# Optimization experiments

Measured on AMD Instinct MI355X. Metric: run time of the kernel, lower is better.

## Reference

```python
import jax, jax.numpy as jnp
import numpy as np

N, E, C_IN, C_OUT, K, D_D = 50000, 800000, 16, 64, 3, 7


def setup_inputs() -> dict:
    key = jax.random.key(0)
    ks = jax.random.split(key, 10)
    s = 0.05
    x = jax.random.normal(ks[0], (N, C_IN), jnp.float32)
    edge_index = jax.random.randint(ks[1], (2, E), 0, N, dtype=jnp.int64)
    edge_weight = jax.random.uniform(ks[2], (E,), jnp.float32)
    h0 = jax.random.normal(ks[3], (N, C_OUT), jnp.float32)
    # stacked ChebConv params: gate order [z, r, h]
    Wx = jax.random.normal(ks[4], (3, K, C_IN, C_OUT), jnp.float32) * s
    Wh = jax.random.normal(ks[5], (3, K, C_OUT, C_OUT), jnp.float32) * s
    bx = jax.random.normal(ks[6], (3, C_OUT), jnp.float32) * s
    bh = jax.random.normal(ks[7], (3, C_OUT), jnp.float32) * s
    Wlin = jax.random.normal(ks[8], (C_OUT, D_D), jnp.float32) * s
    blin = jax.random.normal(ks[9], (D_D,), jnp.float32) * s
    return dict(x=x, edge_index=edge_index, edge_weight=edge_weight, h0=h0,
                Wx=Wx, Wh=Wh, bx=bx, bh=bh, Wlin=Wlin, blin=blin)


def _norm(src, dst, edge_weight, n):
    # ChebConv sym normalization with lambda_max=2:
    # L_sym = I - D^-1/2 A D^-1/2;  L_tilde = 2L/lambda_max - I = -D^-1/2 A D^-1/2
    w = jnp.where(src == dst, 0.0, edge_weight)  # remove self loops
    deg = jax.ops.segment_sum(w, src, num_segments=n)
    dinv = jnp.where(deg > 0, 1.0 / jnp.sqrt(deg), 0.0)
    return -dinv[src] * w * dinv[dst]


def _cheb(t, W, b, src, dst, nw, n):
    # K-hop Chebyshev recursion: Tx_{k+1} = 2*L~*Tx_k - Tx_{k-1}
    prop = lambda v: jax.ops.segment_sum(nw[:, None] * v[src], dst, num_segments=n)
    Tx0 = t
    out = Tx0 @ W[0]
    Tx1 = prop(Tx0)
    out = out + Tx1 @ W[1]
    for k in range(2, W.shape[0]):
        Tx2 = 2.0 * prop(Tx1) - Tx0
        out = out + Tx2 @ W[k]
        Tx0, Tx1 = Tx1, Tx2
    return out + b


def reference(x, edge_index, edge_weight, h0, Wx, Wh, bx, bh, Wlin, blin):
    n = x.shape[0]
    src, dst = edge_index[0], edge_index[1]
    nw = _norm(src, dst, edge_weight, n)
    z = jax.nn.sigmoid(_cheb(x, Wx[0], bx[0], src, dst, nw, n)
                       + _cheb(h0, Wh[0], bh[0], src, dst, nw, n))
    r = jax.nn.sigmoid(_cheb(x, Wx[1], bx[1], src, dst, nw, n)
                       + _cheb(h0, Wh[1], bh[1], src, dst, nw, n))
    htil = jnp.tanh(_cheb(x, Wx[2], bx[2], src, dst, nw, n)
                    + _cheb(h0 * r, Wh[2], bh[2], src, dst, nw, n))
    h = z * h0 + (1.0 - z) * htil
    y = jax.nn.relu(h) @ Wlin + blin
    return (jax.lax.stop_gradient(h), y)
```

## Files before the change

kernel.cpp:

```cpp
#include <hip/hip_runtime.h>

constexpr int NN = 50000;
constexpr int NE = 800000;
constexpr int CI = 16;
constexpr int CO = 64;
constexpr int DD = 7;
constexpr int NXCD = 8;

typedef __bf16 bf16x8 __attribute__((ext_vector_type(8)));
typedef float  f32x4  __attribute__((ext_vector_type(4)));
typedef float  f32x2  __attribute__((ext_vector_type(2)));

__device__ inline float blo(unsigned u) { return __uint_as_float(u << 16); }
__device__ inline float bhi(unsigned u) { return __uint_as_float(u & 0xffff0000u); }

__device__ inline unsigned xcc_id() {
    unsigned v;
    asm volatile("s_getreg_b32 %0, hwreg(HW_REG_XCC_ID)" : "=s"(v));
    return v & 7;
}
__device__ inline int l2_add_ret(int* p, int v) {
    return __hip_atomic_fetch_add(p, v, __ATOMIC_RELAXED, __HIP_MEMORY_SCOPE_WORKGROUP);
}
__device__ inline void l2_add_f(float* p, float v) {
    __hip_atomic_fetch_add(p, v, __ATOMIC_RELAXED, __HIP_MEMORY_SCOPE_WORKGROUP);
}

__device__ inline void acc8_fp8(float acc[8], float w, uint2 u) {
    f32x2 c;
    c = __builtin_amdgcn_cvt_pk_f32_fp8(u.x, false); acc[0] += w * c[0]; acc[1] += w * c[1];
    c = __builtin_amdgcn_cvt_pk_f32_fp8(u.x, true);  acc[2] += w * c[0]; acc[3] += w * c[1];
    c = __builtin_amdgcn_cvt_pk_f32_fp8(u.y, false); acc[4] += w * c[0]; acc[5] += w * c[1];
    c = __builtin_amdgcn_cvt_pk_f32_fp8(u.y, true);  acc[6] += w * c[0]; acc[7] += w * c[1];
}
__device__ inline uint2 pack_fp8x8(const float o[8]) {
    int t0 = __builtin_amdgcn_cvt_pk_fp8_f32(o[0], o[1], 0, false);
    t0 = __builtin_amdgcn_cvt_pk_fp8_f32(o[2], o[3], t0, true);
    int t1 = __builtin_amdgcn_cvt_pk_fp8_f32(o[4], o[5], 0, false);
    t1 = __builtin_amdgcn_cvt_pk_fp8_f32(o[6], o[7], t1, true);
    uint2 r; r.x = (unsigned)t0; r.y = (unsigned)t1; return r;
}
__device__ inline unsigned char fp8_of(float v) {
    return (unsigned char)(__builtin_amdgcn_cvt_pk_fp8_f32(v, v, 0, false) & 0xff);
}


constexpr int EB = (NE + 255) / 256;
constexpr int XOCT = NN * CI / 8;
constexpr int HOCT = NN * CO / 8;
constexpr int CB = (XOCT + HOCT + 255) / 256;

__global__ void __launch_bounds__(256) k_deg_cast_prep(
    const int* __restrict__ src, const int* __restrict__ dst, const float* __restrict__ ew,
    float* __restrict__ deg8, int* __restrict__ count8, uint2* __restrict__ erec,
    const float* __restrict__ x, const float* __restrict__ h0,
    __bf16* __restrict__ x_bf, __bf16* __restrict__ h0_bf, unsigned char* __restrict__ h0_f8,
    const float* __restrict__ Wx, const float* __restrict__ Wh,
    const float* __restrict__ bx, const float* __restrict__ bh,
    bf16x8* __restrict__ BfragZR, bf16x8* __restrict__ BfragHT, float* __restrict__ biasC) {
    int b = blockIdx.x;
    if (b < EB) {
        int e = b * 256 + threadIdx.x;
        if (e >= NE) return;
        int s = src[e], d = dst[e];
        float w = (s == d) ? 0.f : ew[e];
        unsigned xc = xcc_id();
        l2_add_f(&deg8[xc * NN + s], w);
        int rk = l2_add_ret(&count8[xc * NN + d], 1);
        __bf16 wb = (__bf16)w;
        unsigned wu = (unsigned)__builtin_bit_cast(unsigned short, wb);
        erec[e] = make_uint2((unsigned)s | ((unsigned)d << 16),
                             ((unsigned)rk & 0xff) | (xc << 8) | (wu << 16));
    } else if (b < EB + CB) {
        int t = (b - EB) * 256 + threadIdx.x;
        if (t < XOCT) {
            const float* sp = x + (size_t)t * 8;
            float4 a = *(const float4*)sp;
            float4 c = *(const float4*)(sp + 4);
            bf16x8 o;
            o[0] = (__bf16)a.x; o[1] = (__bf16)a.y; o[2] = (__bf16)a.z; o[3] = (__bf16)a.w;
            o[4] = (__bf16)c.x; o[5] = (__bf16)c.y; o[6] = (__bf16)c.z; o[7] = (__bf16)c.w;
            *(bf16x8*)(x_bf + (size_t)t * 8) = o;
        } else if (t < XOCT + HOCT) {
            int u = t - XOCT;
            const float* sp = h0 + (size_t)u * 8;
            float4 a = *(const float4*)sp;
            float4 c = *(const float4*)(sp + 4);
            bf16x8 o;
            o[0] = (__bf16)a.x; o[1] = (__bf16)a.y; o[2] = (__bf16)a.z; o[3] = (__bf16)a.w;
            o[4] = (__bf16)c.x; o[5] = (__bf16)c.y; o[6] = (__bf16)c.z; o[7] = (__bf16)c.w;
            *(bf16x8*)(h0_bf + (size_t)u * 8) = o;
            float f[8] = {a.x, a.y, a.z, a.w, c.x, c.y, c.z, c.w};
            *(uint2*)(h0_f8 + (size_t)u * 8) = pack_fp8x8(f);
        }
    } else {
        int tid = (b - EB - CB) * 256 + threadIdx.x;
        if (tid < 6144) {
            int e = tid, gate, n, kk, l;
            if (e < 4096) {
                int t = e >> 9, rem = e & 511;
                kk = rem >> 6; l = rem & 63;
                n = t * 16 + (l & 15);
                gate = n >> 6;
            } else {
                int e2 = e - 4096;
                int t = e2 >> 9, rem = e2 & 511;
                kk = rem >> 6; l = rem & 63;
                n = t * 16 + (l & 15);
                gate = 2;
            }
            int co = n & 63;
            int k0 = kk * 32 + (l >> 4) * 8;
            bf16x8 f;
#pragma unroll
            for (int j = 0; j < 8; j++) {
                int k = k0 + j;
                float w = 0.f;
                if (k < 48) {
                    int kb = k >> 4, ci = k & 15;
                    const float* Wg = Wx + gate * 3 * 16 * 64;
                    float w0 = Wg[(kb * 16 + ci) * 64 + co];
                    if (kb == 0)      w = w0 - Wg[(2 * 16 + ci) * 64 + co];
                    else if (kb == 1) w = w0;
                    else              w = 2.f * w0;
                } else if (k < 240) {
                    int kh = k - 48, kb = kh >> 6, ci = kh & 63;
                    const float* Wg = Wh + gate * 3 * 64 * 64;
                    float w0 = Wg[(kb * 64 + ci) * 64 + co];
                    if (kb == 0)      w = w0 - Wg[(2 * 64 + ci) * 64 + co];
                    else if (kb == 1) w = w0;
                    else              w = 2.f * w0;
                }
                f[j] = (__bf16)w;
            }
            if (e < 4096) BfragZR[e] = f; else BfragHT[e - 4096] = f;
        } else if (tid < 6144 + 192) {
            int i = tid - 6144;
            biasC[i] = bx[i] + bh[i];
        }
    }
}


__global__ void k_scan1(const int* __restrict__ count8, int* __restrict__ S, int* __restrict__ bsums) {
    __shared__ int ts[256];
    int tid = threadIdx.x;
    int base = blockIdx.x * 1024;
    int vals[4]; int s = 0;
#pragma unroll
    for (int j = 0; j < 4; j++) {
        int idx = base + tid * 4 + j;
        int v = 0;
        if (idx < NN) {
#pragma unroll
            for (int xc = 0; xc < NXCD; xc++) v += count8[xc * NN + idx];
        }
        s += v; vals[j] = s;
    }
    ts[tid] = s;
    __syncthreads();
    for (int off = 1; off < 256; off <<= 1) {
        int v = (tid >= off) ? ts[tid - off] : 0;
        __syncthreads();
        ts[tid] += v;
        __syncthreads();
    }
    int prev = (tid > 0) ? ts[tid - 1] : 0;
#pragma unroll
    for (int j = 0; j < 4; j++) {
        int idx = base + tid * 4 + j;
        if (idx < NN) S[idx] = vals[j] + prev;
    }
    if (tid == 255) bsums[blockIdx.x] = ts[255];
}

__global__ void k_scan23(const int* __restrict__ S, const int* __restrict__ bsums,
                         const int* __restrict__ count8, const float* __restrict__ deg8,
                         int* __restrict__ rowptr, int* __restrict__ off8,
                         float* __restrict__ dinv) {
    int i = blockIdx.x * 256 + threadIdx.x;
    if (i >= NN) return;
    int chunk = blockIdx.x >> 2;
    int pre = 0;
    for (int j = 0; j < chunk; j++) pre += bsums[j];
    int tot = S[i] + pre;
    rowptr[i + 1] = tot;
    if (i == 0) rowptr[0] = 0;
    int c[NXCD]; int ctot = 0;
#pragma unroll
    for (int xc = 0; xc < NXCD; xc++) { c[xc] = count8[xc * NN + i]; ctot += c[xc]; }
    int run = tot - ctot;
#pragma unroll
    for (int xc = 0; xc < NXCD; xc++) { off8[xc * NN + i] = run; run += c[xc]; }
    float dsum = 0.f;
#pragma unroll
    for (int xc = 0; xc < NXCD; xc++) dsum += deg8[xc * NN + i];
    dinv[i] = (dsum > 0.f) ? (1.f / sqrtf(dsum)) : 0.f;
}

__global__ void k_place(const uint2* __restrict__ erec, const float* __restrict__ dinv,
                        const int* __restrict__ off8, unsigned* __restrict__ csr_ew) {
    int e = blockIdx.x * 256 + threadIdx.x;
    if (e >= NE) return;
    uint2 r = erec[e];
    int s = r.x & 0xffff, d = r.x >> 16;
    unsigned rk = r.y & 0xff, xc = (r.y >> 8) & 7;
    float w = bhi(r.y);
    float wp = dinv[s] * w;
    __bf16 wb = (__bf16)wp;
    unsigned short ub = __builtin_bit_cast(unsigned short, wb);
    csr_ew[off8[xc * NN + d] + rk] = (unsigned)s | ((unsigned)ub << 16);
}


__device__ inline void prop64_body(int n, int lane,
                                   const unsigned char* __restrict__ v8,
                                   const float* __restrict__ dinv,
                                   const int* __restrict__ rowptr,
                                   const unsigned* __restrict__ ew,
                                   __bf16* __restrict__ out_bf,
                                   unsigned char* __restrict__ out_f8) {
    int j = lane >> 3, cg = lane & 7;
    int beg = rowptr[n], end = rowptr[n + 1];
    float acc[8] = {0.f, 0.f, 0.f, 0.f, 0.f, 0.f, 0.f, 0.f};
    for (int e = beg + j; e < end; e += 8) {
        unsigned p = ew[e];
        float w = bhi(p);
        int s = p & 0xffff;
        uint2 u = *(const uint2*)(v8 + (size_t)s * 64 + cg * 8);
        acc8_fp8(acc, w, u);
    }
#pragma unroll
    for (int m = 8; m <= 32; m <<= 1) {
#pragma unroll
        for (int i = 0; i < 8; i++) acc[i] += __shfl_xor(acc[i], m, 64);
    }
    if (lane < 8) {
        float f = -dinv[n];
        float o[8];
#pragma unroll
        for (int i = 0; i < 8; i++) o[i] = f * acc[i];
        bf16x8 st;
#pragma unroll
        for (int i = 0; i < 8; i++) st[i] = (__bf16)o[i];
        *(bf16x8*)(out_bf + (size_t)n * 64 + lane * 8) = st;
        if (out_f8) *(uint2*)(out_f8 + (size_t)n * 64 + lane * 8) = pack_fp8x8(o);
    }
}

__device__ inline void prop16_body(int n, int lane,
                                   const __bf16* __restrict__ v,
                                   const float* __restrict__ dinv,
                                   const int* __restrict__ rowptr,
                                   const unsigned* __restrict__ ew, __bf16* __restrict__ out) {
    int j = lane >> 1, cg = lane & 1;
    int beg = rowptr[n], end = rowptr[n + 1];
    float acc[8] = {0.f, 0.f, 0.f, 0.f, 0.f, 0.f, 0.f, 0.f};
    for (int e = beg + j; e < end; e += 32) {
        unsigned p = ew[e];
        float w = bhi(p);
        int s = p & 0xffff;
        uint4 u = *(const uint4*)((const char*)v + ((size_t)s * 32 + cg * 16));
        acc[0] += w * blo(u.x); acc[1] += w * bhi(u.x);
        acc[2] += w * blo(u.y); acc[3] += w * bhi(u.y);
        acc[4] += w * blo(u.z); acc[5] += w * bhi(u.z);
        acc[6] += w * blo(u.w); acc[7] += w * bhi(u.w);
    }
#pragma unroll
    for (int m = 2; m <= 32; m <<= 1) {
#pragma unroll
        for (int i = 0; i < 8; i++) acc[i] += __shfl_xor(acc[i], m, 64);
    }
    if (lane < 2) {
        float f = -dinv[n];
        bf16x8 st;
#pragma unroll
        for (int i = 0; i < 8; i++) st[i] = (__bf16)(f * acc[i]);
        *(bf16x8*)(out + (size_t)n * 16 + lane * 8) = st;
    }
}

__global__ void __launch_bounds__(256) k_stage(
    const unsigned char* __restrict__ vh8, const __bf16* __restrict__ vx,
    const float* __restrict__ dinv,
    const int* __restrict__ rowptr, const unsigned* __restrict__ ew,
    __bf16* __restrict__ outh_bf, unsigned char* __restrict__ outh_f8,
    __bf16* __restrict__ outx) {
    int gw = blockIdx.x * 4 + (threadIdx.x >> 6);
    int lane = threadIdx.x & 63;
    if (gw < NN) prop64_body(gw, lane, vh8, dinv, rowptr, ew, outh_bf, outh_f8);
    else if (gw < 2 * NN) prop16_body(gw - NN, lane, vx, dinv, rowptr, ew, outx);
}

__global__ void __launch_bounds__(256) k_prop64(
    const unsigned char* __restrict__ v8, const float* __restrict__ dinv,
    const int* __restrict__ rowptr, const unsigned* __restrict__ ew,
    __bf16* __restrict__ out_bf, unsigned char* __restrict__ out_f8) {
    int n = blockIdx.x * 4 + (threadIdx.x >> 6);
    if (n >= NN) return;
    prop64_body(n, threadIdx.x & 63, v8, dinv, rowptr, ew, out_bf, out_f8);
}


__device__ inline bf16x8 load_a_bf(int c, int m,
                                   const __bf16* __restrict__ xb, const __bf16* __restrict__ t1,
                                   const __bf16* __restrict__ t2, const __bf16* __restrict__ hb,
                                   const __bf16* __restrict__ h1, const __bf16* __restrict__ h2) {
    if (c >= 30) {
        bf16x8 a;
#pragma unroll
        for (int j = 0; j < 8; j++) a[j] = (__bf16)0.f;
        return a;
    }
    if (c < 6) {
        const __bf16* base = (c < 2) ? xb : ((c < 4) ? t1 : t2);
        return *(const bf16x8*)(base + (size_t)m * 16 + (c & 1) * 8);
    }
    int d = c - 6;
    const __bf16* base = (d < 8) ? hb : ((d < 16) ? h1 : h2);
    return *(const bf16x8*)(base + (size_t)m * 64 + (d & 7) * 8);
}

__global__ void __launch_bounds__(256) k_mfma_zr(
    const __bf16* __restrict__ xb, const __bf16* __restrict__ t1, const __bf16* __restrict__ t2,
    const __bf16* __restrict__ hb, const __bf16* __restrict__ h1, const __bf16* __restrict__ h2,
    const bf16x8* __restrict__ Bfrag, const float* __restrict__ biasC,
    __bf16* __restrict__ z_bf, __bf16* __restrict__ hr_bf, unsigned char* __restrict__ hr_f8) {
    int wv = (blockIdx.x * 256 + threadIdx.x) >> 6;
    if (wv >= NN / 16) return;
    int lane = threadIdx.x & 63;
    int q = lane >> 4, r16 = lane & 15;
    int ma = wv * 16 + r16;
    f32x4 acc[8];
#pragma unroll
    for (int t = 0; t < 8; t++) acc[t] = (f32x4){0.f, 0.f, 0.f, 0.f};
#pragma unroll
    for (int kk = 0; kk < 8; kk++) {
        bf16x8 a = load_a_bf(kk * 4 + q, ma, xb, t1, t2, hb, h1, h2);
#pragma unroll
        for (int t = 0; t < 8; t++)
            acc[t] = __builtin_amdgcn_mfma_f32_16x16x32_bf16(a, Bfrag[(t * 8 + kk) * 64 + lane], acc[t], 0, 0, 0);
    }
    int mbase = wv * 16 + q * 4;
#pragma unroll
    for (int t = 0; t < 8; t++) {
        int co = t * 16 + r16;
        float bias = biasC[co];
        int col = co & 63;
#pragma unroll
        for (int reg = 0; reg < 4; reg++) {
            int mm = mbase + reg;
            float p = acc[t][reg] + bias;
            float s = 1.f / (1.f + __expf(-p));
            if (t < 4) z_bf[(size_t)mm * 64 + col] = (__bf16)s;
            else {
                float hrv = s * (float)hb[(size_t)mm * 64 + col];
                hr_bf[(size_t)mm * 64 + col] = (__bf16)hrv;
                hr_f8[(size_t)mm * 64 + col] = fp8_of(hrv);
            }
        }
    }
}

__global__ void __launch_bounds__(256) k_mfma_ht(
    const __bf16* __restrict__ xb, const __bf16* __restrict__ t1, const __bf16* __restrict__ t2,
    const __bf16* __restrict__ hrb, const __bf16* __restrict__ r1, const __bf16* __restrict__ r2,
    const bf16x8* __restrict__ Bfrag, const float* __restrict__ biasC,
    const __bf16* __restrict__ z_bf, const float* __restrict__ h0,
    const float* __restrict__ Wlin, const float* __restrict__ blin,
    float* __restrict__ hout, float* __restrict__ yout) {
    int wv = (blockIdx.x * 256 + threadIdx.x) >> 6;
    if (wv >= NN / 16) return;
    int lane = threadIdx.x & 63;
    int q = lane >> 4, r16 = lane & 15;
    int ma = wv * 16 + r16;
    f32x4 acc[4];
#pragma unroll
    for (int t = 0; t < 4; t++) acc[t] = (f32x4){0.f, 0.f, 0.f, 0.f};
#pragma unroll
    for (int kk = 0; kk < 8; kk++) {
        bf16x8 a = load_a_bf(kk * 4 + q, ma, xb, t1, t2, hrb, r1, r2);
#pragma unroll
        for (int t = 0; t < 4; t++)
            acc[t] = __builtin_amdgcn_mfma_f32_16x16x32_bf16(a, Bfrag[(t * 8 + kk) * 64 + lane], acc[t], 0, 0, 0);
    }
    int mbase = wv * 16 + q * 4;
    float hbuf[4][4];
#pragma unroll
    for (int t = 0; t < 4; t++) {
        int co = t * 16 + r16;
        float bias = biasC[128 + co];
#pragma unroll
        for (int reg = 0; reg < 4; reg++) {
            int mm = mbase + reg;
            float p = acc[t][reg] + bias;
            float htl = tanhf(p);
            float zv = (float)z_bf[(size_t)mm * 64 + co];
            float h0v = h0[(size_t)mm * 64 + co];
            float hn = zv * h0v + (1.f - zv) * htl;
            hout[(size_t)mm * 64 + co] = hn;
            hbuf[t][reg] = hn;
        }
    }
    float ya[4][DD];
#pragma unroll
    for (int reg = 0; reg < 4; reg++)
#pragma unroll
        for (int d = 0; d < DD; d++) ya[reg][d] = 0.f;
#pragma unroll
    for (int t = 0; t < 4; t++) {
        int cb = (t * 16 + r16) * DD;
        float wl[DD];
#pragma unroll
        for (int d = 0; d < DD; d++) wl[d] = Wlin[cb + d];
#pragma unroll
        for (int reg = 0; reg < 4; reg++) {
            float rh = fmaxf(hbuf[t][reg], 0.f);
#pragma unroll
            for (int d = 0; d < DD; d++) ya[reg][d] += rh * wl[d];
        }
    }
#pragma unroll
    for (int m = 1; m <= 8; m <<= 1) {
#pragma unroll
        for (int reg = 0; reg < 4; reg++)
#pragma unroll
            for (int d = 0; d < DD; d++) ya[reg][d] += __shfl_xor(ya[reg][d], m, 64);
    }
    if (r16 < DD) {
        float b = blin[r16];
#pragma unroll
        for (int reg = 0; reg < 4; reg++) {
            float v = (r16 == 0) ? ya[reg][0] : (r16 == 1) ? ya[reg][1] : (r16 == 2) ? ya[reg][2]
                    : (r16 == 3) ? ya[reg][3] : (r16 == 4) ? ya[reg][4] : (r16 == 5) ? ya[reg][5]
                    : ya[reg][6];
            yout[(size_t)(mbase + reg) * DD + r16] = v + b;
        }
    }
}


extern "C" void kernel_launch(void* const* d_in, const int* in_sizes, int n_in,
                              void* d_out, int out_size, void* d_ws, size_t ws_size,
                              hipStream_t stream) {
    (void)in_sizes; (void)n_in; (void)out_size; (void)ws_size;
    const float* x    = (const float*)d_in[0];
    const int*   eidx = (const int*)d_in[1];
    const float* ew   = (const float*)d_in[2];
    const float* h0   = (const float*)d_in[3];
    const float* Wx   = (const float*)d_in[4];
    const float* Wh   = (const float*)d_in[5];
    const float* bx   = (const float*)d_in[6];
    const float* bh   = (const float*)d_in[7];
    const float* Wlin = (const float*)d_in[8];
    const float* blin = (const float*)d_in[9];
    const int* src = eidx;
    const int* dst = eidx + NE;

    char* ws = (char*)d_ws;
    size_t off = 0;
    auto alloc = [&](size_t nbytes) -> void* {
        void* p = ws + off;
        off += (nbytes + 255) & ~(size_t)255;
        return p;
    };
    float*  deg8    = (float*)alloc((size_t)NXCD * NN * 4);
    int*    count8  = (int*)alloc((size_t)NXCD * NN * 4);
    int*    off8    = (int*)alloc((size_t)NXCD * NN * 4);
    float*  dinv    = (float*)alloc(NN * 4);
    int*    S       = (int*)alloc(NN * 4);
    int*    rowptr  = (int*)alloc((NN + 1) * 4);
    int*    bsums   = (int*)alloc(64 * 4);
    uint2*  erec    = (uint2*)alloc((size_t)NE * 8);
    unsigned* csr_ew = (unsigned*)alloc((size_t)NE * 4);
    __bf16* x_bf    = (__bf16*)alloc((size_t)NN * CI * 2);
    __bf16* h0_bf   = (__bf16*)alloc((size_t)NN * CO * 2);
    unsigned char* h0_f8 = (unsigned char*)alloc((size_t)NN * CO);
    unsigned char* T1_f8 = (unsigned char*)alloc((size_t)NN * CO);
    unsigned char* hr_f8 = (unsigned char*)alloc((size_t)NN * CO);
    __bf16* Tx1     = (__bf16*)alloc((size_t)NN * CI * 2);
    __bf16* Tx2     = (__bf16*)alloc((size_t)NN * CI * 2);
    __bf16* Th1     = (__bf16*)alloc((size_t)NN * CO * 2);
    __bf16* Th2     = (__bf16*)alloc((size_t)NN * CO * 2);
    __bf16* hr_bf   = (__bf16*)alloc((size_t)NN * CO * 2);
    __bf16* z_bf    = (__bf16*)alloc((size_t)NN * CO * 2);
    bf16x8* BfragZR = (bf16x8*)alloc(4096 * 16);
    bf16x8* BfragHT = (bf16x8*)alloc(2048 * 16);
    float*  biasC   = (float*)alloc(192 * 4);

    float* hout = (float*)d_out;
    float* yout = hout + (size_t)NN * CO;

    constexpr int NB = (NN + 1023) / 1024;
    const int NBLK = (NN + 255) / 256;
    const int PROPB = (NN + 3) / 4;
    const int STAGEB = (2 * NN + 3) / 4;
    const int GEMMB = (NN / 16 * 64 + 255) / 256;

    hipMemsetAsync(deg8, 0, (size_t)NXCD * NN * 4, stream);
    hipMemsetAsync(count8, 0, (size_t)NXCD * NN * 4, stream);

    k_deg_cast_prep<<<EB + CB + 25, 256, 0, stream>>>(
        src, dst, ew, deg8, count8, erec, x, h0, x_bf, h0_bf, h0_f8,
        Wx, Wh, bx, bh, BfragZR, BfragHT, biasC);
    k_scan1<<<NB, 256, 0, stream>>>(count8, S, bsums);
    k_scan23<<<NBLK, 256, 0, stream>>>(S, bsums, count8, deg8, rowptr, off8, dinv);
    k_place<<<EB, 256, 0, stream>>>(erec, dinv, off8, csr_ew);

    k_stage<<<STAGEB, 256, 0, stream>>>(h0_f8, x_bf, dinv, rowptr, csr_ew, Th1, T1_f8, Tx1);
    k_stage<<<STAGEB, 256, 0, stream>>>(T1_f8, Tx1, dinv, rowptr, csr_ew, Th2, nullptr, Tx2);

    k_mfma_zr<<<GEMMB, 256, 0, stream>>>(x_bf, Tx1, Tx2, h0_bf, Th1, Th2,
                                         BfragZR, biasC, z_bf, hr_bf, hr_f8);
    k_prop64<<<PROPB, 256, 0, stream>>>(hr_f8, dinv, rowptr, csr_ew, Th1, T1_f8);
    k_prop64<<<PROPB, 256, 0, stream>>>(T1_f8, dinv, rowptr, csr_ew, Th2, nullptr);
    k_mfma_ht<<<GEMMB, 256, 0, stream>>>(x_bf, Tx1, Tx2, hr_bf, Th1, Th2,
                                         BfragHT, biasC, z_bf, h0, Wlin, blin, hout, yout);
}
```

Measured before the change: 363.4 us.

## Build CSR via two-level bucket sort with LDS histograms instead of global atomics

Replaces the per-XCD global-atomic degree/count pass, multi-kernel scan and placement with a counting sort. Edges are first bucketed by node>>8 using per-block shared-memory histograms, a single scan over the bucket tables, and a scatter. Per-bucket kernels then compute degrees and build rowptr/csr with shared-memory atomics. This removes global atomic contention and the memsets, at the cost of more kernels, extra record arrays (drec/srec) and a serial 1024-thread table scan.

```diff
diff --git a/kernel.cpp b/kernel.cpp
--- a/kernel.cpp
+++ b/kernel.cpp
@@ -5,7 +5,11 @@
 constexpr int CI = 16;
 constexpr int CO = 64;
 constexpr int DD = 7;
-constexpr int NXCD = 8;
+
+constexpr int NBUCK = 196;
+constexpr int EPB   = 4096;
+constexpr int NBLK3 = (NE + EPB - 1) / EPB;
+constexpr int TBL   = NBUCK * NBLK3;
 
 typedef __bf16 bf16x8 __attribute__((ext_vector_type(8)));
 typedef float  f32x4  __attribute__((ext_vector_type(4)));
@@ -13,18 +17,6 @@
 
 __device__ inline float blo(unsigned u) { return __uint_as_float(u << 16); }
 __device__ inline float bhi(unsigned u) { return __uint_as_float(u & 0xffff0000u); }
-
-__device__ inline unsigned xcc_id() {
-    unsigned v;
-    asm volatile("s_getreg_b32 %0, hwreg(HW_REG_XCC_ID)" : "=s"(v));
-    return v & 7;
-}
-__device__ inline int l2_add_ret(int* p, int v) {
-    return __hip_atomic_fetch_add(p, v, __ATOMIC_RELAXED, __HIP_MEMORY_SCOPE_WORKGROUP);
-}
-__device__ inline void l2_add_f(float* p, float v) {
-    __hip_atomic_fetch_add(p, v, __ATOMIC_RELAXED, __HIP_MEMORY_SCOPE_WORKGROUP);
-}
 
 __device__ inline void acc8_fp8(float acc[8], float w, uint2 u) {
     f32x2 c;
@@ -45,34 +37,40 @@
 }
 
 
-constexpr int EB = (NE + 255) / 256;
 constexpr int XOCT = NN * CI / 8;
 constexpr int HOCT = NN * CO / 8;
 constexpr int CB = (XOCT + HOCT + 255) / 256;
 
-__global__ void __launch_bounds__(256) k_deg_cast_prep(
-    const int* __restrict__ src, const int* __restrict__ dst, const float* __restrict__ ew,
-    float* __restrict__ deg8, int* __restrict__ count8, uint2* __restrict__ erec,
+__global__ void __launch_bounds__(256) k_count(
+    const int* __restrict__ src, const int* __restrict__ dst,
+    int* __restrict__ Cd, int* __restrict__ Cs,
     const float* __restrict__ x, const float* __restrict__ h0,
     __bf16* __restrict__ x_bf, __bf16* __restrict__ h0_bf, unsigned char* __restrict__ h0_f8,
     const float* __restrict__ Wx, const float* __restrict__ Wh,
     const float* __restrict__ bx, const float* __restrict__ bh,
     bf16x8* __restrict__ BfragZR, bf16x8* __restrict__ BfragHT, float* __restrict__ biasC) {
     int b = blockIdx.x;
-    if (b < EB) {
-        int e = b * 256 + threadIdx.x;
-        if (e >= NE) return;
-        int s = src[e], d = dst[e];
-        float w = (s == d) ? 0.f : ew[e];
-        unsigned xc = xcc_id();
-        l2_add_f(&deg8[xc * NN + s], w);
-        int rk = l2_add_ret(&count8[xc * NN + d], 1);
-        __bf16 wb = (__bf16)w;
-        unsigned wu = (unsigned)__builtin_bit_cast(unsigned short, wb);
-        erec[e] = make_uint2((unsigned)s | ((unsigned)d << 16),
-                             ((unsigned)rk & 0xff) | (xc << 8) | (wu << 16));
-    } else if (b < EB + CB) {
-        int t = (b - EB) * 256 + threadIdx.x;
+    if (b < NBLK3) {
+        __shared__ int hd[NBUCK], hs[NBUCK];
+        for (int i = threadIdx.x; i < NBUCK; i += 256) { hd[i] = 0; hs[i] = 0; }
+        __syncthreads();
+        int base = b * EPB;
+#pragma unroll
+        for (int k = 0; k < EPB / 256; k++) {
+            int e = base + k * 256 + threadIdx.x;
+            if (e < NE) {
+                int s = src[e], d = dst[e];
+                atomicAdd(&hd[d >> 8], 1);
+                atomicAdd(&hs[s >> 8], 1);
+            }
+        }
+        __syncthreads();
+        for (int i = threadIdx.x; i < NBUCK; i += 256) {
+            Cd[i * NBLK3 + b] = hd[i];
+            Cs[i * NBLK3 + b] = hs[i];
+        }
+    } else if (b < NBLK3 + CB) {
+        int t = (b - NBLK3) * 256 + threadIdx.x;
         if (t < XOCT) {
             const float* sp = x + (size_t)t * 8;
             float4 a = *(const float4*)sp;
@@ -94,7 +92,7 @@
             *(uint2*)(h0_f8 + (size_t)u * 8) = pack_fp8x8(f);
         }
     } else {
-        int tid = (b - EB - CB) * 256 + threadIdx.x;
+        int tid = (b - NBLK3 - CB) * 256 + threadIdx.x;
         if (tid < 6144) {
             int e = tid, gate, n, kk, l;
             if (e < 4096) {
@@ -142,74 +140,124 @@
 }
 
 
-__global__ void k_scan1(const int* __restrict__ count8, int* __restrict__ S, int* __restrict__ bsums) {
-    __shared__ int ts[256];
-    int tid = threadIdx.x;
-    int base = blockIdx.x * 1024;
-    int vals[4]; int s = 0;
-#pragma unroll
-    for (int j = 0; j < 4; j++) {
-        int idx = base + tid * 4 + j;
-        int v = 0;
-        if (idx < NN) {
-#pragma unroll
-            for (int xc = 0; xc < NXCD; xc++) v += count8[xc * NN + idx];
-        }
-        s += v; vals[j] = s;
-    }
-    ts[tid] = s;
+__global__ void __launch_bounds__(1024) k_scan_tables(int* __restrict__ Cd, int* __restrict__ Cs) {
+    int* C = (blockIdx.x == 0) ? Cd : Cs;
+    constexpr int CHUNK = (TBL + 1023) / 1024;
+    __shared__ int part[1024];
+    int t = threadIdx.x;
+    int base = t * CHUNK;
+    int v[CHUNK];
+    int s = 0;
+#pragma unroll
+    for (int j = 0; j < CHUNK; j++) {
+        int idx = base + j;
+        int xv = (idx < TBL) ? C[idx] : 0;
+        v[j] = s;
+        s += xv;
+    }
+    part[t] = s;
+    __syncthreads();
+    for (int off = 1; off < 1024; off <<= 1) {
+        int p = (t >= off) ? part[t - off] : 0;
+        __syncthreads();
+        part[t] += p;
+        __syncthreads();
+    }
+    int tb = (t > 0) ? part[t - 1] : 0;
+#pragma unroll
+    for (int j = 0; j < CHUNK; j++) {
+        int idx = base + j;
+        if (idx < TBL) C[idx] = tb + v[j];
+    }
+}
+
+
+__global__ void __launch_bounds__(256) k_scatter(
+    const int* __restrict__ src, const int* __restrict__ dst, const float* __restrict__ ew,
+    const int* __restrict__ Cd, const int* __restrict__ Cs,
+    uint2* __restrict__ drec, uint2* __restrict__ srec) {
+    __shared__ int cd[NBUCK], cs[NBUCK];
+    int b = blockIdx.x;
+    for (int i = threadIdx.x; i < NBUCK; i += 256) {
+        cd[i] = Cd[i * NBLK3 + b];
+        cs[i] = Cs[i * NBLK3 + b];
+    }
+    __syncthreads();
+    int base = b * EPB;
+#pragma unroll
+    for (int k = 0; k < EPB / 256; k++) {
+        int e = base + k * 256 + threadIdx.x;
+        if (e < NE) {
+            int s = src[e], d = dst[e];
+            float w = (s == d) ? 0.f : ew[e];
+            __bf16 wb = (__bf16)w;
+            unsigned wu = (unsigned)__builtin_bit_cast(unsigned short, wb);
+            int pd = atomicAdd(&cd[d >> 8], 1);
+            drec[pd] = make_uint2((unsigned)s | (wu << 16), (unsigned)(d & 255));
+            int ps = atomicAdd(&cs[s >> 8], 1);
+            srec[ps] = make_uint2((unsigned)(s & 255), __builtin_bit_cast(unsigned, w));
+        }
+    }
+}
+
+
+__global__ void __launch_bounds__(256) k_dinv(
+    const int* __restrict__ Cs, const uint2* __restrict__ srec, float* __restrict__ dinv) {
+    int bkt = blockIdx.x;
+    __shared__ float acc[256];
+    acc[threadIdx.x] = 0.f;
+    __syncthreads();
+    int beg = Cs[bkt * NBLK3];
+    int end = (bkt == NBUCK - 1) ? NE : Cs[(bkt + 1) * NBLK3];
+    for (int i = beg + threadIdx.x; i < end; i += 256) {
+        uint2 r = srec[i];
+        atomicAdd(&acc[r.x], __builtin_bit_cast(float, r.y));
+    }
+    __syncthreads();
+    int node = bkt * 256 + threadIdx.x;
+    if (node < NN) {
+        float dsum = acc[threadIdx.x];
+        dinv[node] = (dsum > 0.f) ? (1.f / sqrtf(dsum)) : 0.f;
+    }
+}
+
+
+__global__ void __launch_bounds__(256) k_build(
+    const int* __restrict__ Cd, const uint2* __restrict__ drec, const float* __restrict__ dinv,
+    int* __restrict__ rowptr, unsigned* __restrict__ csr_ew) {
+    int bkt = blockIdx.x;
+    __shared__ int cnt[256], sc[256], cur[256];
+    int t = threadIdx.x;
+    cnt[t] = 0;
+    __syncthreads();
+    int beg = Cd[bkt * NBLK3];
+    int end = (bkt == NBUCK - 1) ? NE : Cd[(bkt + 1) * NBLK3];
+    for (int i = beg + t; i < end; i += 256) atomicAdd(&cnt[drec[i].y], 1);
+    __syncthreads();
+    int val = cnt[t];
+    sc[t] = val;
     __syncthreads();
     for (int off = 1; off < 256; off <<= 1) {
-        int v = (tid >= off) ? ts[tid - off] : 0;
+        int p = (t >= off) ? sc[t - off] : 0;
         __syncthreads();
-        ts[tid] += v;
+        sc[t] += p;
         __syncthreads();
     }
-    int prev = (tid > 0) ? ts[tid - 1] : 0;
-#pragma unroll
-    for (int j = 0; j < 4; j++) {
-        int idx = base + tid * 4 + j;
-        if (idx < NN) S[idx] = vals[j] + prev;
-    }
-    if (tid == 255) bsums[blockIdx.x] = ts[255];
-}
-
-__global__ void k_scan23(const int* __restrict__ S, const int* __restrict__ bsums,
-                         const int* __restrict__ count8, const float* __restrict__ deg8,
-                         int* __restrict__ rowptr, int* __restrict__ off8,
-                         float* __restrict__ dinv) {
-    int i = blockIdx.x * 256 + threadIdx.x;
-    if (i >= NN) return;
-    int chunk = blockIdx.x >> 2;
-    int pre = 0;
-    for (int j = 0; j < chunk; j++) pre += bsums[j];
-    int tot = S[i] + pre;
-    rowptr[i + 1] = tot;
-    if (i == 0) rowptr[0] = 0;
-    int c[NXCD]; int ctot = 0;
-#pragma unroll
-    for (int xc = 0; xc < NXCD; xc++) { c[xc] = count8[xc * NN + i]; ctot += c[xc]; }
-    int run = tot - ctot;
-#pragma unroll
-    for (int xc = 0; xc < NXCD; xc++) { off8[xc * NN + i] = run; run += c[xc]; }
-    float dsum = 0.f;
-#pragma unroll
-    for (int xc = 0; xc < NXCD; xc++) dsum += deg8[xc * NN + i];
-    dinv[i] = (dsum > 0.f) ? (1.f / sqrtf(dsum)) : 0.f;
-}
-
-__global__ void k_place(const uint2* __restrict__ erec, const float* __restrict__ dinv,
-                        const int* __restrict__ off8, unsigned* __restrict__ csr_ew) {
-    int e = blockIdx.x * 256 + threadIdx.x;
-    if (e >= NE) return;
-    uint2 r = erec[e];
-    int s = r.x & 0xffff, d = r.x >> 16;
-    unsigned rk = r.y & 0xff, xc = (r.y >> 8) & 7;
-    float w = bhi(r.y);
-    float wp = dinv[s] * w;
-    __bf16 wb = (__bf16)wp;
-    unsigned short ub = __builtin_bit_cast(unsigned short, wb);
-    csr_ew[off8[xc * NN + d] + rk] = (unsigned)s | ((unsigned)ub << 16);
+    int ex = sc[t] - val;
+    int node = bkt * 256 + t;
+    if (node <= NN) rowptr[node] = beg + ex;
+    cur[t] = ex;
+    __syncthreads();
+    for (int i = beg + t; i < end; i += 256) {
+        uint2 r = drec[i];
+        int slot = beg + atomicAdd(&cur[r.y], 1);
+        unsigned s = r.x & 0xffff;
+        float w = bhi(r.x);
+        float wp = dinv[s] * w;
+        __bf16 wb = (__bf16)wp;
+        unsigned ub = (unsigned)__builtin_bit_cast(unsigned short, wb);
+        csr_ew[slot] = s | (ub << 16);
+    }
 }
 
 
@@ -464,14 +512,12 @@
         off += (nbytes + 255) & ~(size_t)255;
         return p;
     };
-    float*  deg8    = (float*)alloc((size_t)NXCD * NN * 4);
-    int*    count8  = (int*)alloc((size_t)NXCD * NN * 4);
-    int*    off8    = (int*)alloc((size_t)NXCD * NN * 4);
+    int*    Cd      = (int*)alloc((size_t)TBL * 4);
+    int*    Cs      = (int*)alloc((size_t)TBL * 4);
+    uint2*  drec    = (uint2*)alloc((size_t)NE * 8);
+    uint2*  srec    = (uint2*)alloc((size_t)NE * 8);
     float*  dinv    = (float*)alloc(NN * 4);
-    int*    S       = (int*)alloc(NN * 4);
     int*    rowptr  = (int*)alloc((NN + 1) * 4);
-    int*    bsums   = (int*)alloc(64 * 4);
-    uint2*  erec    = (uint2*)alloc((size_t)NE * 8);
     unsigned* csr_ew = (unsigned*)alloc((size_t)NE * 4);
     __bf16* x_bf    = (__bf16*)alloc((size_t)NN * CI * 2);
     __bf16* h0_bf   = (__bf16*)alloc((size_t)NN * CO * 2);
@@ -491,21 +537,17 @@
     float* hout = (float*)d_out;
     float* yout = hout + (size_t)NN * CO;
 
-    constexpr int NB = (NN + 1023) / 1024;
-    const int NBLK = (NN + 255) / 256;
     const int PROPB = (NN + 3) / 4;
     const int STAGEB = (2 * NN + 3) / 4;
     const int GEMMB = (NN / 16 * 64 + 255) / 256;
 
-    hipMemsetAsync(deg8, 0, (size_t)NXCD * NN * 4, stream);
-    hipMemsetAsync(count8, 0, (size_t)NXCD * NN * 4, stream);
-
-    k_deg_cast_prep<<<EB + CB + 25, 256, 0, stream>>>(
-        src, dst, ew, deg8, count8, erec, x, h0, x_bf, h0_bf, h0_f8,
+    k_count<<<NBLK3 + CB + 25, 256, 0, stream>>>(
+        src, dst, Cd, Cs, x, h0, x_bf, h0_bf, h0_f8,
         Wx, Wh, bx, bh, BfragZR, BfragHT, biasC);
-    k_scan1<<<NB, 256, 0, stream>>>(count8, S, bsums);
-    k_scan23<<<NBLK, 256, 0, stream>>>(S, bsums, count8, deg8, rowptr, off8, dinv);
-    k_place<<<EB, 256, 0, stream>>>(erec, dinv, off8, csr_ew);
+    k_scan_tables<<<2, 1024, 0, stream>>>(Cd, Cs);
+    k_scatter<<<NBLK3, 256, 0, stream>>>(src, dst, ew, Cd, Cs, drec, srec);
+    k_dinv<<<NBUCK, 256, 0, stream>>>(Cs, srec, dinv);
+    k_build<<<NBUCK, 256, 0, stream>>>(Cd, drec, dinv, rowptr, csr_ew);
 
     k_stage<<<STAGEB, 256, 0, stream>>>(h0_f8, x_bf, dinv, rowptr, csr_ew, Th1, T1_f8, Tx1);
     k_stage<<<STAGEB, 256, 0, stream>>>(T1_f8, Tx1, dinv, rowptr, csr_ew, Th2, nullptr, Tx2);
```

New measurement: 334.8 us. 1.09x faster.
